# Optimization experiments

Measured on AMD Instinct MI355X. Metric: run time of the kernel, lower is better.

The kernel has to match this reference:

```python
import jax, jax.numpy as jnp
import numpy as np
import math

T, B, D, M = 512, 8, 512, 128

def setup_inputs() -> dict:
    key = jax.random.key(0)
    ks = jax.random.split(key, 16)
    def xav(k, shape):
        fan_in, fan_out = shape[0], shape[1]
        a = math.sqrt(6.0 / (fan_in + fan_out))
        return jax.random.uniform(k, shape, jnp.float32, -a, a)
    return {
        "x": jax.random.normal(ks[0], (T, B, D), jnp.float32),
        "C_prev": jax.random.normal(ks[1], (T, B, M, M), jnp.float32) * 0.1,
        "n_prev": jax.random.normal(ks[2], (T, B, M), jnp.float32) * 0.1,
        "Wq": xav(ks[3], (D, M)), "bq": xav(ks[4], (1, M)),
        "Wk": xav(ks[5], (D, M)), "bk": xav(ks[6], (1, M)),
        "Wv": xav(ks[7], (D, M)), "bv": xav(ks[8], (1, M)),
        "wi": xav(ks[9], (D, 1)), "bi": jnp.zeros((1,), jnp.float32),
        "wf": xav(ks[10], (D, 1)), "bf": jnp.zeros((1,), jnp.float32),
        "Wo": xav(ks[11], (D, M)), "bo": xav(ks[12], (1, M)),
    }

def reference(x, C_prev, n_prev, Wq, bq, Wk, bk, Wv, bv, wi, bi, wf, bf, Wo, bo):
    mem_dim = Wq.shape[1]
    qt = x @ Wq + bq                                      # (T,B,M)
    kt = (x @ Wk + bk) * (1.0 / math.sqrt(mem_dim))       # (T,B,M)
    vt = x @ Wv + bv                                      # (T,B,M)
    it = jnp.exp(x @ wi + bi)[..., None]                  # (T,B,1,1)
    ft = jax.nn.sigmoid(x @ wf + bf)[..., None]           # (T,B,1,1)
    # gated rank-1 outer-product state update
    C = ft * C_prev + it * (vt[..., :, None] * kt[..., None, :])  # (T,B,M,M)
    n = ft[..., 0] * n_prev + it[..., 0] * kt             # (T,B,M)
    # max(|n . q|, 1) normalizer
    max_nqt = jnp.maximum(jnp.abs(jnp.sum(n * qt, axis=-1, keepdims=True)), 1.0)  # (T,B,1)
    h_tilde = jnp.einsum('tbij,tbj->tbi', C, qt) / max_nqt  # (T,B,M)
    ot = jax.nn.sigmoid(x @ Wo + bo)                      # (T,B,M)
    ht = ot * h_tilde
    return (ht, C, n)
```

## Files before the change

kernel.cpp:

```cpp
#include <hip/hip_runtime.h>
#include <math.h>

constexpr int kT = 512;
constexpr int kB = 8;
constexpr int kD = 512;
constexpr int kM = 128;
constexpr int kNPairs = kT * kB;
constexpr int kGP = 8;
constexpr int kThreads = 256;
constexpr int kRB = 64;

typedef float f32x4 __attribute__((ext_vector_type(4)));
typedef float f32x2 __attribute__((ext_vector_type(2)));

__global__ __launch_bounds__(kThreads)
void mlstm_gates(const float* __restrict__ x,
                 const float* __restrict__ n_prev,
                 const float* __restrict__ Wq, const float* __restrict__ bq,
                 const float* __restrict__ Wk, const float* __restrict__ bk,
                 const float* __restrict__ Wv, const float* __restrict__ bv,
                 const float* __restrict__ wi, const float* __restrict__ bi,
                 const float* __restrict__ wf, const float* __restrict__ bf,
                 const float* __restrict__ Wo, const float* __restrict__ bo,
                 float* __restrict__ gq, float* __restrict__ gk,
                 float* __restrict__ gv, float* __restrict__ go,
                 float* __restrict__ gi, float* __restrict__ gf,
                 float* __restrict__ ginv,
                 float* __restrict__ out_n)
{
    __shared__ float sq[kGP][kM];
    __shared__ float sk[kGP][kM];
    __shared__ float sif[kGP][2];

    const int tid = threadIdx.x;
    const int w   = tid >> 6;
    const int l   = tid & 63;
    const int pair_base = blockIdx.x * kGP;
    const float* __restrict__ xblk = x + (size_t)pair_base * kD;

    {
        const float* __restrict__ Wm = (w == 0) ? Wq : (w == 1) ? Wk : (w == 2) ? Wv : Wo;
        const float* __restrict__ bm = (w == 0) ? bq : (w == 1) ? bk : (w == 2) ? bv : bo;

        f32x2 acc[kGP];
        #pragma unroll
        for (int p = 0; p < kGP; ++p) acc[p] = (f32x2){0.f, 0.f};

        const int c = 2 * l;

        #pragma unroll 4
        for (int d = 0; d < kD; ++d) {
            const f32x2 w2 = *reinterpret_cast<const f32x2*>(Wm + d * kM + c);
            #pragma unroll
            for (int p = 0; p < kGP; ++p) {
                const float xv = xblk[p * kD + d];
                const f32x2 xx = {xv, xv};
                acc[p] += xx * w2;
            }
        }

        const f32x2 b2 = *reinterpret_cast<const f32x2*>(bm + c);
        const float inv_sqrt_m = 0.08838834764831845f;
        float* __restrict__ gm = (w == 0) ? gq : (w == 1) ? gk : (w == 2) ? gv : go;

        #pragma unroll
        for (int p = 0; p < kGP; ++p) {
            f32x2 v = acc[p] + b2;
            if (w == 1) { v.x *= inv_sqrt_m; v.y *= inv_sqrt_m; }
            if (w == 3) {
                v.x = 1.f / (1.f + expf(-v.x));
                v.y = 1.f / (1.f + expf(-v.y));
            }
            *reinterpret_cast<f32x2*>(gm + (size_t)(pair_base + p) * kM + c) = v;
            if (w == 0) *reinterpret_cast<f32x2*>(&sq[p][c]) = v;
            if (w == 1) *reinterpret_cast<f32x2*>(&sk[p][c]) = v;
        }
    }

    {
        const int p = 2 * w + (l >> 5);
        const int s = l & 31;
        float ip = 0.f, fp = 0.f;
        #pragma unroll
        for (int dd = 0; dd < kD / 32; ++dd) {
            const int d = s + 32 * dd;
            const float xv = xblk[p * kD + d];
            ip += xv * wi[d];
            fp += xv * wf[d];
        }
        #pragma unroll
        for (int msk = 16; msk >= 1; msk >>= 1) {
            ip += __shfl_xor(ip, msk, 64);
            fp += __shfl_xor(fp, msk, 64);
        }
        if (s == 0) {
            sif[p][0] = expf(ip + bi[0]);
            sif[p][1] = 1.f / (1.f + expf(-(fp + bf[0])));
        }
    }
    __syncthreads();

    {
        const int p = tid >> 5;
        const int s = tid & 31;
        const size_t pi = (size_t)(pair_base + p);
        const float iv = sif[p][0];
        const float fv = sif[p][1];

        const float4 np4 = *reinterpret_cast<const float4*>(n_prev + pi * kM + 4 * s);
        const float4 k4  = *reinterpret_cast<const float4*>(&sk[p][4 * s]);
        const float4 q4  = *reinterpret_cast<const float4*>(&sq[p][4 * s]);

        float4 n4;
        n4.x = fv * np4.x + iv * k4.x;
        n4.y = fv * np4.y + iv * k4.y;
        n4.z = fv * np4.z + iv * k4.z;
        n4.w = fv * np4.w + iv * k4.w;
        *reinterpret_cast<float4*>(out_n + pi * kM + 4 * s) = n4;

        float nq = n4.x * q4.x + n4.y * q4.y + n4.z * q4.z + n4.w * q4.w;
        nq += __shfl_xor(nq, 16, 64);
        nq += __shfl_xor(nq, 8, 64);
        nq += __shfl_xor(nq, 4, 64);
        nq += __shfl_xor(nq, 2, 64);
        nq += __shfl_xor(nq, 1, 64);
        if (s == 0) {
            gi[pi]   = iv;
            gf[pi]   = fv;
            ginv[pi] = 1.f / fmaxf(fabsf(nq), 1.0f);
        }
    }
}

__global__ __launch_bounds__(kThreads)
void mlstm_stream(const float* __restrict__ C_prev,
                  const float* __restrict__ gq, const float* __restrict__ gk,
                  const float* __restrict__ gv, const float* __restrict__ go,
                  const float* __restrict__ gi, const float* __restrict__ gf,
                  const float* __restrict__ ginv,
                  float* __restrict__ out_C,
                  float* __restrict__ out_ht)
{
    const int pair = blockIdx.x >> 1;
    const int rblk = (blockIdx.x & 1) * kRB;
    const int tid  = threadIdx.x;
    const int r0   = tid >> 5;
    const int s    = tid & 31;

    __shared__ float sv_s[kRB];
    __shared__ float sh_s[kRB];

    if (tid < kRB / 4)
        reinterpret_cast<float4*>(sv_s)[tid] =
            reinterpret_cast<const float4*>(gv + (size_t)pair * kM + rblk)[tid];

    const float iv = gi[pair];
    const float fv = gf[pair];
    const float4 k4 = *reinterpret_cast<const float4*>(gk + (size_t)pair * kM + 4 * s);
    const float4 q4 = *reinterpret_cast<const float4*>(gq + (size_t)pair * kM + 4 * s);
    __syncthreads();

    const size_t cbase = (size_t)pair * (kM * kM) + (size_t)rblk * kM;
    const f32x4* cp = reinterpret_cast<const f32x4*>(C_prev + cbase);
    f32x4*       cn = reinterpret_cast<f32x4*>(out_C + cbase);

    f32x4 c4[8];
    #pragma unroll
    for (int j = 0; j < 8; ++j)
        c4[j] = cp[tid + kThreads * j];

    float hpart[8];
    #pragma unroll
    for (int j = 0; j < 8; ++j) {
        const int r = r0 + 8 * j;
        const float ivr = iv * sv_s[r];
        f32x4 c_new;
        c_new.x = fv * c4[j].x + ivr * k4.x;
        c_new.y = fv * c4[j].y + ivr * k4.y;
        c_new.z = fv * c4[j].z + ivr * k4.z;
        c_new.w = fv * c4[j].w + ivr * k4.w;
        __builtin_nontemporal_store(c_new, &cn[tid + kThreads * j]);
        hpart[j] = c_new.x * q4.x + c_new.y * q4.y
                 + c_new.z * q4.z + c_new.w * q4.w;
    }

    #pragma unroll
    for (int j = 0; j < 8; ++j) {
        float v = hpart[j];
        v += __shfl_xor(v, 16, 64);
        v += __shfl_xor(v, 8, 64);
        v += __shfl_xor(v, 4, 64);
        v += __shfl_xor(v, 2, 64);
        v += __shfl_xor(v, 1, 64);
        if (s == 0) sh_s[r0 + 8 * j] = v;
    }
    __syncthreads();

    if (tid < kRB / 4) {
        const float inv = ginv[pair];
        const float4 h4 = reinterpret_cast<const float4*>(sh_s)[tid];
        const float4 o4 = reinterpret_cast<const float4*>(go + (size_t)pair * kM + rblk)[tid];
        float4 ht4;
        ht4.x = o4.x * h4.x * inv;
        ht4.y = o4.y * h4.y * inv;
        ht4.z = o4.z * h4.z * inv;
        ht4.w = o4.w * h4.w * inv;
        reinterpret_cast<float4*>(out_ht + (size_t)pair * kM + rblk)[tid] = ht4;
    }
}

extern "C" void kernel_launch(void* const* d_in, const int* in_sizes, int n_in,
                              void* d_out, int out_size, void* d_ws, size_t ws_size,
                              hipStream_t stream) {
    const float* x      = (const float*)d_in[0];
    const float* C_prev = (const float*)d_in[1];
    const float* n_prev = (const float*)d_in[2];
    const float* Wq = (const float*)d_in[3];
    const float* bq = (const float*)d_in[4];
    const float* Wk = (const float*)d_in[5];
    const float* bk = (const float*)d_in[6];
    const float* Wv = (const float*)d_in[7];
    const float* bv = (const float*)d_in[8];
    const float* wi = (const float*)d_in[9];
    const float* bi = (const float*)d_in[10];
    const float* wf = (const float*)d_in[11];
    const float* bf = (const float*)d_in[12];
    const float* Wo = (const float*)d_in[13];
    const float* bo = (const float*)d_in[14];

    float* out    = (float*)d_out;
    float* out_ht = out;
    float* out_C  = out + (size_t)kNPairs * kM;
    float* out_n  = out_C + (size_t)kNPairs * kM * kM;

    float* ws = (float*)d_ws;
    const size_t gsz = (size_t)kNPairs * kM;
    float* gq   = ws;
    float* gk   = gq + gsz;
    float* gv   = gk + gsz;
    float* go   = gv + gsz;
    float* gi   = go + gsz;
    float* gf   = gi + kNPairs;
    float* ginv = gf + kNPairs;

    mlstm_gates<<<dim3(kNPairs / kGP), dim3(kThreads), 0, stream>>>(
        x, n_prev, Wq, bq, Wk, bk, Wv, bv, wi, bi, wf, bf, Wo, bo,
        gq, gk, gv, go, gi, gf, ginv, out_n);

    mlstm_stream<<<dim3(kNPairs * (kM / kRB)), dim3(kThreads), 0, stream>>>(
        C_prev, gq, gk, gv, go, gi, gf, ginv, out_C, out_ht);
}
```

Baseline: 144.5 us.

## Split gate projection K dimension across two thread halves with LDS reduction

The gates kernel doubles to 512 threads, and each projection matrix's D=512 reduction is split between two groups of four waves. Partial sums meet through a new shared-memory buffer. The i/f gate dot products are redistributed so each wave handles one pair. In the stream kernel, all C updates are computed before the nontemporal stores are issued. The goals are shorter serial reduction chains and more latency hiding, at the cost of an extra barrier, shared-memory traffic and possible register pressure under the larger launch bound.

After: 188.1 us. +30.2%, slower.

```diff
diff --git a/kernel.cpp b/kernel.cpp
--- a/kernel.cpp
+++ b/kernel.cpp
@@ -7,13 +7,14 @@
 constexpr int kM = 128;
 constexpr int kNPairs = kT * kB;
 constexpr int kGP = 8;
+constexpr int kGateThreads = 512;
 constexpr int kThreads = 256;
 constexpr int kRB = 64;
 
 typedef float f32x4 __attribute__((ext_vector_type(4)));
 typedef float f32x2 __attribute__((ext_vector_type(2)));
 
-__global__ __launch_bounds__(kThreads)
+__global__ __launch_bounds__(kGateThreads)
 void mlstm_gates(const float* __restrict__ x,
                  const float* __restrict__ n_prev,
                  const float* __restrict__ Wq, const float* __restrict__ bq,
@@ -30,77 +31,90 @@
 {
     __shared__ float sq[kGP][kM];
     __shared__ float sk[kGP][kM];
+    __shared__ float sacc[4][kGP][kM];
     __shared__ float sif[kGP][2];
 
     const int tid = threadIdx.x;
     const int w   = tid >> 6;
+    const int m   = w & 3;
+    const int dh  = w >> 2;
     const int l   = tid & 63;
     const int pair_base = blockIdx.x * kGP;
     const float* __restrict__ xblk = x + (size_t)pair_base * kD;
 
+    const float* __restrict__ Wm = (m == 0) ? Wq : (m == 1) ? Wk : (m == 2) ? Wv : Wo;
+    const float* __restrict__ bm = (m == 0) ? bq : (m == 1) ? bk : (m == 2) ? bv : bo;
+
+    const int c = 2 * l;
+
+    f32x2 acc[kGP];
+    #pragma unroll
+    for (int p = 0; p < kGP; ++p) acc[p] = (f32x2){0.f, 0.f};
+
     {
-        const float* __restrict__ Wm = (w == 0) ? Wq : (w == 1) ? Wk : (w == 2) ? Wv : Wo;
-        const float* __restrict__ bm = (w == 0) ? bq : (w == 1) ? bk : (w == 2) ? bv : bo;
-
-        f32x2 acc[kGP];
-        #pragma unroll
-        for (int p = 0; p < kGP; ++p) acc[p] = (f32x2){0.f, 0.f};
-
-        const int c = 2 * l;
-
+        const float* __restrict__ Wh = Wm + (size_t)(dh * (kD / 2)) * kM;
+        const float* __restrict__ xh = xblk + dh * (kD / 2);
         #pragma unroll 4
-        for (int d = 0; d < kD; ++d) {
-            const f32x2 w2 = *reinterpret_cast<const f32x2*>(Wm + d * kM + c);
+        for (int d = 0; d < kD / 2; ++d) {
+            const f32x2 w2 = *reinterpret_cast<const f32x2*>(Wh + d * kM + c);
             #pragma unroll
             for (int p = 0; p < kGP; ++p) {
-                const float xv = xblk[p * kD + d];
+                const float xv = xh[p * kD + d];
                 const f32x2 xx = {xv, xv};
                 acc[p] += xx * w2;
             }
         }
-
+    }
+
+    if (dh == 1) {
+        #pragma unroll
+        for (int p = 0; p < kGP; ++p)
+            *reinterpret_cast<f32x2*>(&sacc[m][p][c]) = acc[p];
+    }
+    __syncthreads();
+
+    if (dh == 0) {
         const f32x2 b2 = *reinterpret_cast<const f32x2*>(bm + c);
         const float inv_sqrt_m = 0.08838834764831845f;
-        float* __restrict__ gm = (w == 0) ? gq : (w == 1) ? gk : (w == 2) ? gv : go;
+        float* __restrict__ gm = (m == 0) ? gq : (m == 1) ? gk : (m == 2) ? gv : go;
 
         #pragma unroll
         for (int p = 0; p < kGP; ++p) {
-            f32x2 v = acc[p] + b2;
-            if (w == 1) { v.x *= inv_sqrt_m; v.y *= inv_sqrt_m; }
-            if (w == 3) {
+            f32x2 v = acc[p] + *reinterpret_cast<const f32x2*>(&sacc[m][p][c]) + b2;
+            if (m == 1) { v.x *= inv_sqrt_m; v.y *= inv_sqrt_m; }
+            if (m == 3) {
                 v.x = 1.f / (1.f + expf(-v.x));
                 v.y = 1.f / (1.f + expf(-v.y));
             }
             *reinterpret_cast<f32x2*>(gm + (size_t)(pair_base + p) * kM + c) = v;
-            if (w == 0) *reinterpret_cast<f32x2*>(&sq[p][c]) = v;
-            if (w == 1) *reinterpret_cast<f32x2*>(&sk[p][c]) = v;
+            if (m == 0) *reinterpret_cast<f32x2*>(&sq[p][c]) = v;
+            if (m == 1) *reinterpret_cast<f32x2*>(&sk[p][c]) = v;
         }
     }
 
     {
-        const int p = 2 * w + (l >> 5);
-        const int s = l & 31;
+        const int p = w;
         float ip = 0.f, fp = 0.f;
         #pragma unroll
-        for (int dd = 0; dd < kD / 32; ++dd) {
-            const int d = s + 32 * dd;
+        for (int dd = 0; dd < kD / 64; ++dd) {
+            const int d = l + 64 * dd;
             const float xv = xblk[p * kD + d];
             ip += xv * wi[d];
             fp += xv * wf[d];
         }
         #pragma unroll
-        for (int msk = 16; msk >= 1; msk >>= 1) {
+        for (int msk = 32; msk >= 1; msk >>= 1) {
             ip += __shfl_xor(ip, msk, 64);
             fp += __shfl_xor(fp, msk, 64);
         }
-        if (s == 0) {
+        if (l == 0) {
             sif[p][0] = expf(ip + bi[0]);
             sif[p][1] = 1.f / (1.f + expf(-(fp + bf[0])));
         }
     }
     __syncthreads();
 
-    {
+    if (tid < 32 * kGP) {
         const int p = tid >> 5;
         const int s = tid & 31;
         const size_t pi = (size_t)(pair_base + p);
@@ -174,15 +188,17 @@
     for (int j = 0; j < 8; ++j) {
         const int r = r0 + 8 * j;
         const float ivr = iv * sv_s[r];
-        f32x4 c_new;
-        c_new.x = fv * c4[j].x + ivr * k4.x;
-        c_new.y = fv * c4[j].y + ivr * k4.y;
-        c_new.z = fv * c4[j].z + ivr * k4.z;
-        c_new.w = fv * c4[j].w + ivr * k4.w;
-        __builtin_nontemporal_store(c_new, &cn[tid + kThreads * j]);
-        hpart[j] = c_new.x * q4.x + c_new.y * q4.y
-                 + c_new.z * q4.z + c_new.w * q4.w;
-    }
+        c4[j].x = fv * c4[j].x + ivr * k4.x;
+        c4[j].y = fv * c4[j].y + ivr * k4.y;
+        c4[j].z = fv * c4[j].z + ivr * k4.z;
+        c4[j].w = fv * c4[j].w + ivr * k4.w;
+        hpart[j] = c4[j].x * q4.x + c4[j].y * q4.y
+                 + c4[j].z * q4.z + c4[j].w * q4.w;
+    }
+
+    #pragma unroll
+    for (int j = 0; j < 8; ++j)
+        __builtin_nontemporal_store(c4[j], &cn[tid + kThreads * j]);
 
     #pragma unroll
     for (int j = 0; j < 8; ++j) {
@@ -243,7 +259,7 @@
     float* gf   = gi + kNPairs;
     float* ginv = gf + kNPairs;
 
-    mlstm_gates<<<dim3(kNPairs / kGP), dim3(kThreads), 0, stream>>>(
+    mlstm_gates<<<dim3(kNPairs / kGP), dim3(kGateThreads), 0, stream>>>(
         x, n_prev, Wq, bq, Wk, bk, Wv, bv, wi, bi, wf, bf, Wo, bo,
         gq, gk, gv, go, gi, gf, ginv, out_n);
 
```
